# Kernel tuning notes

Hardware: AMD Instinct MI355X
Metric: run time of the kernel (lower is better)

Reference implementation:

```python
import jax, jax.numpy as jnp
import numpy as np

B, S, D, H, DFF = 8, 1024, 1024, 16, 4096
DK = D // H
EPS = 1e-6
NEG = -1e9


def _layer_norm(x, gamma, beta):
    # Faithful to hand-rolled LN: torch std is unbiased (ddof=1), eps added to sigma.
    mu = jnp.mean(x, axis=-1, keepdims=True)
    sigma = jnp.std(x, axis=-1, keepdims=True, ddof=1)
    return gamma * (x - mu) / (EPS + sigma) + beta


def setup_inputs() -> dict:
    key = jax.random.key(0)
    ks = jax.random.split(key, 12)
    s = 0.02
    inp = {
        "x": jax.random.normal(ks[0], (B, S, D), dtype=jnp.float32),
        "src_mask": jnp.ones((B, 1, 1, S), dtype=jnp.int32),
        "Wq": jax.random.normal(ks[1], (D, D), dtype=jnp.float32) * s,
        "bq": jnp.zeros((D,), dtype=jnp.float32),
        "Wk": jax.random.normal(ks[2], (D, D), dtype=jnp.float32) * s,
        "bk": jnp.zeros((D,), dtype=jnp.float32),
        "Wv": jax.random.normal(ks[3], (D, D), dtype=jnp.float32) * s,
        "bv": jnp.zeros((D,), dtype=jnp.float32),
        "Wo": jax.random.normal(ks[4], (D, D), dtype=jnp.float32) * s,
        "bo": jnp.zeros((D,), dtype=jnp.float32),
        "W1": jax.random.normal(ks[5], (DFF, D), dtype=jnp.float32) * s,
        "b1": jnp.zeros((DFF,), dtype=jnp.float32),
        "W2": jax.random.normal(ks[6], (D, DFF), dtype=jnp.float32) * s,
        "b2": jnp.zeros((D,), dtype=jnp.float32),
        "g1": jnp.ones((1,), dtype=jnp.float32),
        "be1": jnp.zeros((1,), dtype=jnp.float32),
        "g2": jnp.ones((1,), dtype=jnp.float32),
        "be2": jnp.zeros((1,), dtype=jnp.float32),
    }
    return inp


def _encoder_block(x, src_mask, Wq, bq, Wk, bk, Wv, bv, Wo, bo,
                   W1, b1, W2, b2, g1, be1, g2, be2):
    # Multi-head self-attention (dropout = identity in eval)
    def split(h):  # [B,S,D] -> [B,H,S,DK]
        return h.reshape(B, S, H, DK).transpose(0, 2, 1, 3)

    q = split(x @ Wq.T + bq)
    k = split(x @ Wk.T + bk)
    v = split(x @ Wv.T + bv)

    scores = jnp.einsum("bhqd,bhkd->bhqk", q, k) / jnp.sqrt(jnp.float32(DK))
    scores = jnp.where(src_mask == 0, NEG, scores)
    probs = jax.nn.softmax(scores, axis=-1)
    attn = jnp.einsum("bhqk,bhkd->bhqd", probs, v)
    attn = attn.transpose(0, 2, 1, 3).reshape(B, S, D)
    attn = attn @ Wo.T + bo

    x1 = _layer_norm(x + attn, g1, be1)

    ff = jax.nn.relu(x1 @ W1.T + b1) @ W2.T + b2
    x2 = _layer_norm(x1 + ff, g2, be2)
    return x2


def reference(x, src_mask, Wq, bq, Wk, bk, Wv, bv, Wo, bo,
              W1, b1, W2, b2, g1, be1, g2, be2):
    return _encoder_block(x, src_mask, Wq, bq, Wk, bk, Wv, bv, Wo, bo,
                          W1, b1, W2, b2, g1, be1, g2, be2)
```

## Files before the change

### kernel.cpp

```cpp
#include <hip/hip_runtime.h>
#include <stdint.h>

#define BB 8
#define SS 1024
#define DD 1024
#define HH 16
#define DFF 4096
#define MT (BB*SS)

typedef __attribute__((ext_vector_type(8))) short bf16x8;
typedef __attribute__((ext_vector_type(4))) short s16x4;
typedef __attribute__((ext_vector_type(4))) float f32x4;
typedef __attribute__((ext_vector_type(16))) float f32x16;
typedef unsigned int u32x2 __attribute__((ext_vector_type(2)));

#define LOG2E 1.44269504088896340736f

__device__ __forceinline__ short f2bf(float f) {
  union { float f; uint32_t u; } v; v.f = f;
  uint32_t r = v.u + 0x7FFFu + ((v.u >> 16) & 1u);
  return (short)(r >> 16);
}

__device__ __forceinline__ void gload_lds16(const void* g, void* l) {
  __builtin_amdgcn_global_load_lds(
      (__attribute__((address_space(1))) uint32_t*)(uintptr_t)g,
      (__attribute__((address_space(3))) uint32_t*)(uint32_t)(uintptr_t)l,
      16, 0, 0);
}

__device__ __forceinline__ uint32_t cvtpk(float lo, float hi) {
  uint32_t r;
  asm("v_cvt_pk_bf16_f32 %0, %1, %2" : "=v"(r) : "v"(lo), "v"(hi));
  return r;
}

__device__ __forceinline__ void swap2(uint32_t a, uint32_t b, uint32_t& x, uint32_t& y) {
#if __has_builtin(__builtin_amdgcn_permlane32_swap)
  u32x2 r = __builtin_amdgcn_permlane32_swap(a, b, false, false);
  x = r.x; y = r.y;
#else
  uint32_t asw = (uint32_t)__shfl_xor((int)a, 32, 64);
  uint32_t bsw = (uint32_t)__shfl_xor((int)b, 32, 64);
  bool h = (threadIdx.x & 32) != 0;
  x = h ? bsw : a;
  y = h ? b : asw;
#endif
}

__global__ __launch_bounds__(256) void cvt_bf16(const float* __restrict__ in,
                                                short* __restrict__ out, int n8) {
  int i = blockIdx.x * 256 + threadIdx.x;
  if (i >= n8) return;
  f32x4 a = *(const f32x4*)(in + (size_t)i * 8);
  f32x4 b = *(const f32x4*)(in + (size_t)i * 8 + 4);
  bf16x8 o;
  o[0]=f2bf(a[0]); o[1]=f2bf(a[1]); o[2]=f2bf(a[2]); o[3]=f2bf(a[3]);
  o[4]=f2bf(b[0]); o[5]=f2bf(b[1]); o[6]=f2bf(b[2]); o[7]=f2bf(b[3]);
  *(bf16x8*)(out + (size_t)i * 8) = o;
}

template<int RELU, int RES, int OUTF, int OUTB>
__global__ __launch_bounds__(256) void gemm_nt(
    const short* __restrict__ A, const short* __restrict__ W,
    const float* __restrict__ bias, const float* __restrict__ res,
    float* __restrict__ outF, short* __restrict__ outB,
    int M, int N, int K)
{
  __shared__ short As[128 * 64];
  __shared__ short Bs[128 * 64];
  const int tid = threadIdx.x, lane = tid & 63, wid = tid >> 6;
  const int wm = wid >> 1, wn = wid & 1;
  const int lrow = lane & 15, lk = lane >> 4;
  const int row0 = blockIdx.y * 128;
  const int col0 = blockIdx.x * 128;

  const f32x4 z4 = {0.f, 0.f, 0.f, 0.f};
  f32x4 acc[4][4];
#pragma unroll
  for (int i = 0; i < 4; ++i)
#pragma unroll
    for (int j = 0; j < 4; ++j) acc[i][j] = z4;

  const int srow = tid >> 3;
  const int su = (tid & 7) ^ (srow & 7);
  const short* Abase = A + (size_t)(row0 + srow) * K + su * 8;
  const short* Wbase = W + (size_t)(col0 + srow) * K + su * 8;

  for (int kt = 0; kt < K; kt += 64) {
#pragma unroll
    for (int i = 0; i < 4; ++i) {
      gload_lds16(Abase + (size_t)i * 32 * K + kt, As + (i * 256 + wid * 64) * 8);
      gload_lds16(Wbase + (size_t)i * 32 * K + kt, Bs + (i * 256 + wid * 64) * 8);
    }
    __syncthreads();
#pragma unroll
    for (int kk = 0; kk < 2; ++kk) {
      bf16x8 af[4], bfr[4];
#pragma unroll
      for (int mi = 0; mi < 4; ++mi) {
        int row = wm * 64 + mi * 16 + lrow;
        af[mi] = *(const bf16x8*)(As + row * 64 + (((kk * 4 + lk) ^ (row & 7)) * 8));
      }
#pragma unroll
      for (int ni = 0; ni < 4; ++ni) {
        int row = wn * 64 + ni * 16 + lrow;
        bfr[ni] = *(const bf16x8*)(Bs + row * 64 + (((kk * 4 + lk) ^ (row & 7)) * 8));
      }
#pragma unroll
      for (int mi = 0; mi < 4; ++mi)
#pragma unroll
        for (int ni = 0; ni < 4; ++ni)
          acc[mi][ni] = __builtin_amdgcn_mfma_f32_16x16x32_bf16(af[mi], bfr[ni], acc[mi][ni], 0, 0, 0);
    }
    __syncthreads();
  }

#pragma unroll
  for (int mi = 0; mi < 4; ++mi) {
#pragma unroll
    for (int ni = 0; ni < 4; ++ni) {
      int col = col0 + wn * 64 + ni * 16 + lrow;
      float bv = bias[col];
#pragma unroll
      for (int r = 0; r < 4; ++r) {
        int row = row0 + wm * 64 + mi * 16 + lk * 4 + r;
        float v = acc[mi][ni][r] + bv;
        if (RELU) v = fmaxf(v, 0.f);
        size_t idx = (size_t)row * N + col;
        if (RES)  v += res[idx];
        if (OUTF) outF[idx] = v;
        if (OUTB) outB[idx] = f2bf(v);
      }
    }
  }
}

__global__ __launch_bounds__(256) void transpose_v(const short* __restrict__ Vb,
                                                   short* __restrict__ Vt) {
  const int s = blockIdx.x * 256 + threadIdx.x;
  const int u = blockIdx.y;
  const int bh = blockIdx.z, b = bh >> 4, h = bh & 15;
  bf16x8 v = *(const bf16x8*)(Vb + ((size_t)(b * SS + s)) * DD + h * 64 + u * 8);
  size_t ob = ((size_t)bh * 64 + u * 8) * SS + s;
#pragma unroll
  for (int j = 0; j < 8; ++j) Vt[ob + (size_t)j * SS] = v[j];
}

__global__ __launch_bounds__(256) void attn_flash2(
    const short* __restrict__ Qm, const short* __restrict__ Km,
    const short* __restrict__ Vtg, const int* __restrict__ mask,
    short* __restrict__ Om)
{
  __shared__ short Ks[64 * 64];
  __shared__ short Vs[64 * 64];
  __shared__ float ma[64];
  __shared__ float fb[4 * 32];

  const int tid = threadIdx.x, lane = tid & 63, wid = tid >> 6;
  const int l31 = lane & 31, hi = lane >> 5;
  const int bh = blockIdx.y, b = bh >> 4, h = bh & 15;
  const int q0 = blockIdx.x * 128 + wid * 32;

  bf16x8 qf[4];
  {
    const short* qrow = Qm + ((size_t)(b * SS + q0 + l31)) * DD + h * 64;
#pragma unroll
    for (int t = 0; t < 4; ++t) qf[t] = *(const bf16x8*)(qrow + t * 16 + hi * 8);
  }

  f32x16 acc0, acc1;
#pragma unroll
  for (int i = 0; i < 16; ++i) { acc0[i] = 0.f; acc1[i] = 0.f; }
  float m_r = -3e38f, l_r = 0.f;

  const int srow = tid >> 3;
  const int su = tid & 7;

  for (int kt = 0; kt < SS; kt += 64) {
    __syncthreads();
#pragma unroll
    for (int i = 0; i < 2; ++i) {
      int r = i * 32 + srow;
      int uu = su ^ (r & 7);
      gload_lds16(Km + ((size_t)(b * SS + kt + r)) * DD + h * 64 + uu * 8,
                  Ks + i * 2048 + wid * 512);
      gload_lds16(Vtg + ((size_t)(bh * 64 + r)) * SS + kt + uu * 8,
                  Vs + i * 2048 + wid * 512);
    }
    if (tid < 64) ma[tid] = (mask[b * SS + kt + tid] == 0) ? -1e9f : 0.f;
    __syncthreads();

    f32x16 s0, s1;
#pragma unroll
    for (int i = 0; i < 16; ++i) { s0[i] = 0.f; s1[i] = 0.f; }
#pragma unroll
    for (int t = 0; t < 4; ++t) {
      int u = (t * 2 + hi) ^ (l31 & 7);
      bf16x8 k0 = *(const bf16x8*)(Ks + l31 * 64 + u * 8);
      bf16x8 k1 = *(const bf16x8*)(Ks + (32 + l31) * 64 + u * 8);
      s0 = __builtin_amdgcn_mfma_f32_32x32x16_bf16(k0, qf[t], s0, 0, 0, 0);
      s1 = __builtin_amdgcn_mfma_f32_32x32x16_bf16(k1, qf[t], s1, 0, 0, 0);
    }

    float p0[16], p1[16];
    float mx = -3e38f;
#pragma unroll
    for (int g = 0; g < 4; ++g) {
      f32x4 a0 = *(const f32x4*)(ma + g * 8 + hi * 4);
      f32x4 a1 = *(const f32x4*)(ma + 32 + g * 8 + hi * 4);
#pragma unroll
      for (int j = 0; j < 4; ++j) {
        float v0 = s0[g * 4 + j] * 0.125f + a0[j];
        float v1 = s1[g * 4 + j] * 0.125f + a1[j];
        p0[g * 4 + j] = v0; p1[g * 4 + j] = v1;
        mx = fmaxf(mx, fmaxf(v0, v1));
      }
    }
    mx = fmaxf(mx, __shfl_xor(mx, 32, 64));
    float mn  = fmaxf(m_r, mx);
    float fac = exp2f((m_r - mn) * LOG2E);
    m_r = mn;
    float mnl = mn * LOG2E;
    float rs = 0.f;
#pragma unroll
    for (int r = 0; r < 16; ++r) {
      p0[r] = exp2f(p0[r] * LOG2E - mnl);
      p1[r] = exp2f(p1[r] * LOG2E - mnl);
      rs += p0[r] + p1[r];
    }
    rs += __shfl_xor(rs, 32, 64);
    l_r = l_r * fac + rs;

    fb[wid * 32 + l31] = fac;
#pragma unroll
    for (int g = 0; g < 4; ++g) {
      f32x4 fv = *(const f32x4*)(fb + wid * 32 + g * 8 + hi * 4);
#pragma unroll
      for (int j = 0; j < 4; ++j) { acc0[g * 4 + j] *= fv[j]; acc1[g * 4 + j] *= fv[j]; }
    }

    uint32_t w0[8], w1[8];
#pragma unroll
    for (int m = 0; m < 8; ++m) {
      w0[m] = cvtpk(p0[2 * m], p0[2 * m + 1]);
      w1[m] = cvtpk(p1[2 * m], p1[2 * m + 1]);
    }
    uint32_t pa[4][4];
    swap2(w0[0], w0[2], pa[0][0], pa[0][2]);
    swap2(w0[1], w0[3], pa[0][1], pa[0][3]);
    swap2(w0[4], w0[6], pa[1][0], pa[1][2]);
    swap2(w0[5], w0[7], pa[1][1], pa[1][3]);
    swap2(w1[0], w1[2], pa[2][0], pa[2][2]);
    swap2(w1[1], w1[3], pa[2][1], pa[2][3]);
    swap2(w1[4], w1[6], pa[3][0], pa[3][2]);
    swap2(w1[5], w1[7], pa[3][1], pa[3][3]);

#pragma unroll
    for (int kc = 0; kc < 4; ++kc) {
      union { uint32_t w[4]; bf16x8 v; } pu;
      pu.w[0] = pa[kc][0]; pu.w[1] = pa[kc][1]; pu.w[2] = pa[kc][2]; pu.w[3] = pa[kc][3];
      int u = (kc * 2 + hi) ^ (l31 & 7);
      bf16x8 v0 = *(const bf16x8*)(Vs + l31 * 64 + u * 8);
      bf16x8 v1 = *(const bf16x8*)(Vs + (32 + l31) * 64 + u * 8);
      acc0 = __builtin_amdgcn_mfma_f32_32x32x16_bf16(pu.v, v0, acc0, 0, 0, 0);
      acc1 = __builtin_amdgcn_mfma_f32_32x32x16_bf16(pu.v, v1, acc1, 0, 0, 0);
    }
  }

  fb[wid * 32 + l31] = 1.f / l_r;
#pragma unroll
  for (int g = 0; g < 4; ++g) {
    f32x4 rv = *(const f32x4*)(fb + wid * 32 + g * 8 + hi * 4);
#pragma unroll
    for (int j = 0; j < 4; ++j) {
      int q = q0 + g * 8 + hi * 4 + j;
      size_t base = ((size_t)(b * SS + q)) * DD + h * 64 + l31;
      Om[base]      = f2bf(acc0[g * 4 + j] * rv[j]);
      Om[base + 32] = f2bf(acc1[g * 4 + j] * rv[j]);
    }
  }
}

template<int WRITE_BF16>
__global__ __launch_bounds__(256) void layernorm_k(
    float* __restrict__ x, short* __restrict__ xb,
    const float* __restrict__ g, const float* __restrict__ be)
{
  const int row = blockIdx.x, tid = threadIdx.x;
  float* xr = x + (size_t)row * DD;
  f32x4 a = *(const f32x4*)(xr + tid * 4);
  float s  = a[0] + a[1] + a[2] + a[3];
  float ss = a[0]*a[0] + a[1]*a[1] + a[2]*a[2] + a[3]*a[3];
#pragma unroll
  for (int o = 1; o < 64; o <<= 1) { s += __shfl_xor(s, o, 64); ss += __shfl_xor(ss, o, 64); }
  __shared__ float red[8];
  const int wid = tid >> 6, lane = tid & 63;
  if (lane == 0) { red[wid] = s; red[4 + wid] = ss; }
  __syncthreads();
  s  = red[0] + red[1] + red[2] + red[3];
  ss = red[4] + red[5] + red[6] + red[7];
  float mu  = s * (1.f / DD);
  float var = fmaxf((ss - (float)DD * mu * mu) * (1.f / (DD - 1)), 0.f);
  float inv = g[0] / (1e-6f + sqrtf(var));
  float bb  = be[0];
#pragma unroll
  for (int j = 0; j < 4; ++j) a[j] = (a[j] - mu) * inv + bb;
  *(f32x4*)(xr + tid * 4) = a;
  if (WRITE_BF16) {
    s16x4 o;
#pragma unroll
    for (int j = 0; j < 4; ++j) o[j] = f2bf(a[j]);
    *(s16x4*)(xb + (size_t)row * DD + tid * 4) = o;
  }
}

extern "C" void kernel_launch(void* const* d_in, const int* in_sizes, int n_in,
                              void* d_out, int out_size, void* d_ws, size_t ws_size,
                              hipStream_t stream) {
  const float* x    = (const float*)d_in[0];
  const int*   mask = (const int*)d_in[1];
  const float* Wq = (const float*)d_in[2];  const float* bq = (const float*)d_in[3];
  const float* Wk = (const float*)d_in[4];  const float* bk = (const float*)d_in[5];
  const float* Wv = (const float*)d_in[6];  const float* bv = (const float*)d_in[7];
  const float* Wo = (const float*)d_in[8];  const float* bo = (const float*)d_in[9];
  const float* W1 = (const float*)d_in[10]; const float* b1 = (const float*)d_in[11];
  const float* W2 = (const float*)d_in[12]; const float* b2 = (const float*)d_in[13];
  const float* g1 = (const float*)d_in[14]; const float* be1 = (const float*)d_in[15];
  const float* g2 = (const float*)d_in[16]; const float* be2 = (const float*)d_in[17];
  float* out = (float*)d_out;

  char* ws = (char*)d_ws;
  size_t off = 0;
  auto alloc = [&](size_t bytes) -> char* {
    char* p = ws + off; off += (bytes + 255) & ~(size_t)255; return p;
  };
  short* xb  = (short*)alloc((size_t)MT * DD * 2);
  short* wqb = (short*)alloc((size_t)DD * DD * 2);
  short* wkb = (short*)alloc((size_t)DD * DD * 2);
  short* wvb = (short*)alloc((size_t)DD * DD * 2);
  short* wob = (short*)alloc((size_t)DD * DD * 2);
  short* w1b = (short*)alloc((size_t)DFF * DD * 2);
  short* w2b = (short*)alloc((size_t)DD * DFF * 2);
  short* Qb  = (short*)alloc((size_t)MT * DD * 2);
  short* Kb  = (short*)alloc((size_t)MT * DD * 2);
  short* Vb  = (short*)alloc((size_t)MT * DD * 2);
  short* Ab  = (short*)alloc((size_t)MT * DD * 2);
  float* x1  = (float*)alloc((size_t)MT * DD * 4);
  short* F1  = Qb;
  short* x1b = xb;
  short* Vt  = (short*)x1;

  cvt_bf16<<<(MT * DD / 8 + 255) / 256, 256, 0, stream>>>(x, xb, MT * DD / 8);
  cvt_bf16<<<(DD * DD / 8 + 255) / 256, 256, 0, stream>>>(Wq, wqb, DD * DD / 8);
  cvt_bf16<<<(DD * DD / 8 + 255) / 256, 256, 0, stream>>>(Wk, wkb, DD * DD / 8);
  cvt_bf16<<<(DD * DD / 8 + 255) / 256, 256, 0, stream>>>(Wv, wvb, DD * DD / 8);
  cvt_bf16<<<(DD * DD / 8 + 255) / 256, 256, 0, stream>>>(Wo, wob, DD * DD / 8);
  cvt_bf16<<<(DFF * DD / 8 + 255) / 256, 256, 0, stream>>>(W1, w1b, DFF * DD / 8);
  cvt_bf16<<<(DD * DFF / 8 + 255) / 256, 256, 0, stream>>>(W2, w2b, DD * DFF / 8);

  gemm_nt<0,0,0,1><<<dim3(DD/128, MT/128), 256, 0, stream>>>(xb, wqb, bq, nullptr, nullptr, Qb, MT, DD, DD);
  gemm_nt<0,0,0,1><<<dim3(DD/128, MT/128), 256, 0, stream>>>(xb, wkb, bk, nullptr, nullptr, Kb, MT, DD, DD);
  gemm_nt<0,0,0,1><<<dim3(DD/128, MT/128), 256, 0, stream>>>(xb, wvb, bv, nullptr, nullptr, Vb, MT, DD, DD);

  transpose_v<<<dim3(SS/256, 8, BB*HH), 256, 0, stream>>>(Vb, Vt);
  attn_flash2<<<dim3(SS/128, BB*HH), 256, 0, stream>>>(Qb, Kb, Vt, mask, Ab);

  gemm_nt<0,1,1,0><<<dim3(DD/128, MT/128), 256, 0, stream>>>(Ab, wob, bo, x, x1, nullptr, MT, DD, DD);
  layernorm_k<1><<<MT, 256, 0, stream>>>(x1, x1b, g1, be1);

  gemm_nt<1,0,0,1><<<dim3(DFF/128, MT/128), 256, 0, stream>>>(x1b, w1b, b1, nullptr, nullptr, F1, MT, DFF, DD);
  gemm_nt<0,1,1,0><<<dim3(DD/128, MT/128), 256, 0, stream>>>(F1, w2b, b2, x1, out, nullptr, MT, DD, DFF);
  layernorm_k<0><<<MT, 256, 0, stream>>>(out, nullptr, g2, be2);
}
```

Before: 436.0 us.

## Replace GEMM with triple-buffered ring pipeline, larger tiles, fused QKV launch

Rewrites the NT GEMM as a 512-thread kernel with a three-slot LDS ring. Global-to-LDS loads for tile t+2 are issued while tile t is computed, with partial vmcnt waits instead of full syncs, and MFMA runs at raised priority. Tiles grow to 256x256 or 128x256, and workgroup IDs are remapped across 8 groups for locality. The Q/K/V projections become one N=3072 launch that relies on the weight and output buffers being contiguous. The gain targets GEMM latency hiding and launch count, at the cost of more LDS and registers and a dependence on allocation layout.

```diff
diff --git a/kernel.cpp b/kernel.cpp
--- a/kernel.cpp
+++ b/kernel.cpp
@@ -60,77 +60,123 @@
   *(bf16x8*)(out + (size_t)i * 8) = o;
 }
 
-template<int RELU, int RES, int OUTF, int OUTB>
-__global__ __launch_bounds__(256) void gemm_nt(
+template<int BM, int RELU, int RES, int OUTF, int OUTB, int QKV>
+__global__ __launch_bounds__(512, 2) void gemm_ring(
     const short* __restrict__ A, const short* __restrict__ W,
-    const float* __restrict__ bias, const float* __restrict__ res,
+    const float* __restrict__ bq, const float* __restrict__ bk,
+    const float* __restrict__ bv, const float* __restrict__ res,
     float* __restrict__ outF, short* __restrict__ outB,
     int M, int N, int K)
 {
-  __shared__ short As[128 * 64];
-  __shared__ short Bs[128 * 64];
+  constexpr int AISS   = BM / 128;
+  constexpr int SLOT_A = BM * 32 * 2;
+  constexpr int SLOT   = SLOT_A + 256 * 32 * 2;
+  constexpr int MI     = BM / 32;
+  __shared__ __align__(16) char lds[3 * SLOT];
+
   const int tid = threadIdx.x, lane = tid & 63, wid = tid >> 6;
-  const int wm = wid >> 1, wn = wid & 1;
+  const int wm = wid >> 2, wn = wid & 3;
   const int lrow = lane & 15, lk = lane >> 4;
-  const int row0 = blockIdx.y * 128;
-  const int col0 = blockIdx.x * 128;
+
+  const int nwg = gridDim.x;
+  const int cpx = nwg >> 3;
+  const int id  = blockIdx.x;
+  const int wg  = (id & 7) * cpx + (id >> 3);
+  const int gx  = N >> 8;
+  const int bx  = wg % gx, by = wg / gx;
+  const int row0 = by * BM, col0 = bx * 256;
+
+  const int lineo = lane >> 3;
+  const int rin   = lineo * 2 + ((lane >> 2) & 1);
+  const int ksrc  = (lane & 3) ^ (lineo & 3);
+
+  const short* Asrc[AISS];
+#pragma unroll
+  for (int j = 0; j < AISS; ++j)
+    Asrc[j] = A + (size_t)(row0 + (wid * AISS + j) * 16 + rin) * K + ksrc * 8;
+  const short* Bsrc[2];
+#pragma unroll
+  for (int j = 0; j < 2; ++j)
+    Bsrc[j] = W + (size_t)(col0 + (wid * 2 + j) * 16 + rin) * K + ksrc * 8;
 
   const f32x4 z4 = {0.f, 0.f, 0.f, 0.f};
-  f32x4 acc[4][4];
-#pragma unroll
-  for (int i = 0; i < 4; ++i)
+  f32x4 acc[MI][4];
+#pragma unroll
+  for (int i = 0; i < MI; ++i)
 #pragma unroll
     for (int j = 0; j < 4; ++j) acc[i][j] = z4;
 
-  const int srow = tid >> 3;
-  const int su = (tid & 7) ^ (srow & 7);
-  const short* Abase = A + (size_t)(row0 + srow) * K + su * 8;
-  const short* Wbase = W + (size_t)(col0 + srow) * K + su * 8;
-
-  for (int kt = 0; kt < K; kt += 64) {
-#pragma unroll
-    for (int i = 0; i < 4; ++i) {
-      gload_lds16(Abase + (size_t)i * 32 * K + kt, As + (i * 256 + wid * 64) * 8);
-      gload_lds16(Wbase + (size_t)i * 32 * K + kt, Bs + (i * 256 + wid * 64) * 8);
-    }
-    __syncthreads();
-#pragma unroll
-    for (int kk = 0; kk < 2; ++kk) {
-      bf16x8 af[4], bfr[4];
-#pragma unroll
-      for (int mi = 0; mi < 4; ++mi) {
-        int row = wm * 64 + mi * 16 + lrow;
-        af[mi] = *(const bf16x8*)(As + row * 64 + (((kk * 4 + lk) ^ (row & 7)) * 8));
-      }
-#pragma unroll
-      for (int ni = 0; ni < 4; ++ni) {
-        int row = wn * 64 + ni * 16 + lrow;
-        bfr[ni] = *(const bf16x8*)(Bs + row * 64 + (((kk * 4 + lk) ^ (row & 7)) * 8));
-      }
-#pragma unroll
-      for (int mi = 0; mi < 4; ++mi)
-#pragma unroll
-        for (int ni = 0; ni < 4; ++ni)
-          acc[mi][ni] = __builtin_amdgcn_mfma_f32_16x16x32_bf16(af[mi], bfr[ni], acc[mi][ni], 0, 0, 0);
-    }
-    __syncthreads();
-  }
-
-#pragma unroll
-  for (int mi = 0; mi < 4; ++mi) {
+  const int NT = K >> 5;
+
+  auto stage = [&](int ts, int s) {
+    char* base = lds + s * SLOT;
+    int ko = ts * 32;
+#pragma unroll
+    for (int j = 0; j < AISS; ++j)
+      gload_lds16(Asrc[j] + ko, base + (wid * AISS + j) * 1024);
+#pragma unroll
+    for (int j = 0; j < 2; ++j)
+      gload_lds16(Bsrc[j] + ko, base + SLOT_A + (wid * 2 + j) * 1024);
+  };
+
+  stage(0, 0);
+  stage(1, 1);
+
+  const int laneterm = (lrow >> 1) * 128 + (lrow & 1) * 64 + ((lk ^ ((lrow >> 1) & 3)) * 16);
+
+  int sr = 0;
+  for (int t = 0; t < NT; ++t) {
+    const int sw = (sr == 0) ? 2 : sr - 1;
+    const int ts = (t + 2 < NT) ? t + 2 : NT - 1;
+    stage(ts, sw);
+    if (AISS == 2) asm volatile("s_waitcnt vmcnt(8)" ::: "memory");
+    else           asm volatile("s_waitcnt vmcnt(6)" ::: "memory");
+    __builtin_amdgcn_s_barrier();
+    __builtin_amdgcn_sched_barrier(0);
+
+    const char* As = lds + sr * SLOT;
+    const char* Bs = As + SLOT_A;
+    bf16x8 af[MI], bfr[4];
+#pragma unroll
+    for (int mi = 0; mi < MI; ++mi)
+      af[mi] = *(const bf16x8*)(As + wm * (BM * 32) + mi * 1024 + laneterm);
+#pragma unroll
+    for (int ni = 0; ni < 4; ++ni)
+      bfr[ni] = *(const bf16x8*)(Bs + wn * 4096 + ni * 1024 + laneterm);
+
+    __builtin_amdgcn_s_setprio(1);
+#pragma unroll
+    for (int mi = 0; mi < MI; ++mi)
+#pragma unroll
+      for (int ni = 0; ni < 4; ++ni)
+        acc[mi][ni] = __builtin_amdgcn_mfma_f32_16x16x32_bf16(af[mi], bfr[ni], acc[mi][ni], 0, 0, 0);
+    __builtin_amdgcn_s_setprio(0);
+
+    __builtin_amdgcn_s_barrier();
+    sr = (sr == 2) ? 0 : sr + 1;
+  }
+
+  const int sel    = QKV ? (col0 >> 10) : 0;
+  const float* bias = QKV ? (sel == 0 ? bq : (sel == 1 ? bk : bv)) : bq;
+  const int strideN = QKV ? 1024 : N;
+  short* outBp = OUTB ? (outB + (QKV ? (size_t)sel * MT * DD : 0)) : outB;
+
+#pragma unroll
+  for (int mi = 0; mi < MI; ++mi) {
 #pragma unroll
     for (int ni = 0; ni < 4; ++ni) {
-      int col = col0 + wn * 64 + ni * 16 + lrow;
-      float bv = bias[col];
+      int col  = col0 + wn * 64 + ni * 16 + lrow;
+      int coll = QKV ? (col & 1023) : col;
+      float bvv = bias[coll];
 #pragma unroll
       for (int r = 0; r < 4; ++r) {
-        int row = row0 + wm * 64 + mi * 16 + lk * 4 + r;
-        float v = acc[mi][ni][r] + bv;
+        int row = row0 + wm * (BM / 2) + mi * 16 + lk * 4 + r;
+        float v = acc[mi][ni][r] + bvv;
         if (RELU) v = fmaxf(v, 0.f);
-        size_t idx = (size_t)row * N + col;
+        size_t idx = (size_t)row * strideN + coll;
         if (RES)  v += res[idx];
         if (OUTF) outF[idx] = v;
-        if (OUTB) outB[idx] = f2bf(v);
+        if (OUTB) outBp[idx] = f2bf(v);
       }
     }
   }
@@ -350,6 +396,7 @@
   short* F1  = Qb;
   short* x1b = xb;
   short* Vt  = (short*)x1;
+  (void)wkb; (void)wvb; (void)Kb; (void)Vb;
 
   cvt_bf16<<<(MT * DD / 8 + 255) / 256, 256, 0, stream>>>(x, xb, MT * DD / 8);
   cvt_bf16<<<(DD * DD / 8 + 255) / 256, 256, 0, stream>>>(Wq, wqb, DD * DD / 8);
@@ -359,17 +406,19 @@
   cvt_bf16<<<(DFF * DD / 8 + 255) / 256, 256, 0, stream>>>(W1, w1b, DFF * DD / 8);
   cvt_bf16<<<(DD * DFF / 8 + 255) / 256, 256, 0, stream>>>(W2, w2b, DD * DFF / 8);
 
-  gemm_nt<0,0,0,1><<<dim3(DD/128, MT/128), 256, 0, stream>>>(xb, wqb, bq, nullptr, nullptr, Qb, MT, DD, DD);
-  gemm_nt<0,0,0,1><<<dim3(DD/128, MT/128), 256, 0, stream>>>(xb, wkb, bk, nullptr, nullptr, Kb, MT, DD, DD);
-  gemm_nt<0,0,0,1><<<dim3(DD/128, MT/128), 256, 0, stream>>>(xb, wvb, bv, nullptr, nullptr, Vb, MT, DD, DD);
+  gemm_ring<256,0,0,0,1,1><<<dim3((3072/256)*(MT/256)), 512, 0, stream>>>(
+      xb, wqb, bq, bk, bv, nullptr, nullptr, Qb, MT, 3072, DD);
 
   transpose_v<<<dim3(SS/256, 8, BB*HH), 256, 0, stream>>>(Vb, Vt);
   attn_flash2<<<dim3(SS/128, BB*HH), 256, 0, stream>>>(Qb, Kb, Vt, mask, Ab);
 
-  gemm_nt<0,1,1,0><<<dim3(DD/128, MT/128), 256, 0, stream>>>(Ab, wob, bo, x, x1, nullptr, MT, DD, DD);
+  gemm_ring<128,0,1,1,0,0><<<dim3((DD/256)*(MT/128)), 512, 0, stream>>>(
+      Ab, wob, bo, bo, bo, x, x1, nullptr, MT, DD, DD);
   layernorm_k<1><<<MT, 256, 0, stream>>>(x1, x1b, g1, be1);
 
-  gemm_nt<1,0,0,1><<<dim3(DFF/128, MT/128), 256, 0, stream>>>(x1b, w1b, b1, nullptr, nullptr, F1, MT, DFF, DD);
-  gemm_nt<0,1,1,0><<<dim3(DD/128, MT/128), 256, 0, stream>>>(F1, w2b, b2, x1, out, nullptr, MT, DD, DFF);
+  gemm_ring<256,1,0,0,1,0><<<dim3((DFF/256)*(MT/256)), 512, 0, stream>>>(
+      x1b, w1b, b1, b1, b1, nullptr, nullptr, F1, MT, DFF, DD);
+  gemm_ring<128,0,1,1,0,0><<<dim3((DD/256)*(MT/128)), 512, 0, stream>>>(
+      F1, w2b, b2, b2, b2, x1, out, nullptr, MT, DD, DFF);
   layernorm_k<0><<<MT, 256, 0, stream>>>(out, nullptr, g2, be2);
 }
```

Measured after the change: 400.8 us. -8.1%, faster.
